# Kernel optimization log

Measured on AMD Instinct MI355X. Metric: run time of the kernel, lower is better.

## Reference

```python
import jax, jax.numpy as jnp
import numpy as np

D_MODEL = 4096
RANK = 16
BATCH = 4
SEQ = 4096


def setup_inputs() -> dict:
    key = jax.random.key(0)
    k_x, k_w, k_b, k_a, k_bb = jax.random.split(key, 5)
    x = jax.random.normal(k_x, (BATCH, SEQ, D_MODEL), dtype=jnp.float32)
    W = jax.random.normal(k_w, (D_MODEL, D_MODEL), dtype=jnp.float32) * 0.02
    bias = jax.random.normal(k_b, (D_MODEL,), dtype=jnp.float32) * 0.02
    A = jax.random.normal(k_a, (D_MODEL, RANK), dtype=jnp.float32) * 0.01
    B = jax.random.normal(k_bb, (RANK, D_MODEL), dtype=jnp.float32) * 0.01
    return {"x": x, "W": W, "bias": bias, "A": A, "B": B}


def reference(x, W, bias, A, B):
    # Faithful to the torch module: delta_W = A @ B; linear(x, W + delta_W, bias)
    # i.e. out = x @ (W + A @ B)^T + bias, with W: [d_out, d_in], x: [b, s, d_in].
    delta_W = A @ B                                   # [d_out, d_in]
    out = jnp.einsum("bsi,oi->bso", x, W + delta_W) + bias
    return out
```

## Files before the change

### kernel.cpp

```cpp
#include <hip/hip_runtime.h>
#include <stdint.h>


#define MDIM 16384
#define NDIM 4096
#define KDIM 4096
#define RANK 16
#define NT   (KDIM / 64)

typedef __bf16  bf16x8 __attribute__((ext_vector_type(8)));
typedef float   f32x4  __attribute__((ext_vector_type(4)));
typedef unsigned short u16x8 __attribute__((ext_vector_type(8)));

__device__ __forceinline__ unsigned short f2bf(float f) {
  union { float f; uint32_t u; } v; v.f = f;
  uint32_t r = v.u + 0x7FFFu + ((v.u >> 16) & 1u);
  return (unsigned short)(r >> 16);
}

__device__ __forceinline__ void gl16(const void* g, void* l) {
  __builtin_amdgcn_global_load_lds(
      (__attribute__((address_space(1))) void*)(g),
      (__attribute__((address_space(3))) void*)(l),
      16, 0, 0);
}

#define CAST_BLOCKS 32768
__global__ void prep_fused(const float* __restrict__ x,
                           const float* __restrict__ W,
                           const float* __restrict__ A,
                           const float* __restrict__ Bm,
                           unsigned short* __restrict__ xb,
                           unsigned short* __restrict__ Wp) {
  const int b = blockIdx.x;
  if (b < CAST_BLOCKS) {
    const size_t i = ((size_t)b * 256 + threadIdx.x) * 8;
    float4 a0 = *(const float4*)(x + i);
    float4 a1 = *(const float4*)(x + i + 4);
    u16x8 o;
    o[0] = f2bf(a0.x); o[1] = f2bf(a0.y); o[2] = f2bf(a0.z); o[3] = f2bf(a0.w);
    o[4] = f2bf(a1.x); o[5] = f2bf(a1.y); o[6] = f2bf(a1.z); o[7] = f2bf(a1.w);
    *(u16x8*)(xb + i) = o;
  } else {
    const size_t idx = ((size_t)(b - CAST_BLOCKS) * 256 + threadIdx.x) * 8;
    const int o  = (int)(idx >> 12);
    const int i0 = (int)(idx & 4095);
    float accv[8];
    {
      float4 w0 = *(const float4*)(W + (size_t)o * NDIM + i0);
      float4 w1 = *(const float4*)(W + (size_t)o * NDIM + i0 + 4);
      accv[0] = w0.x; accv[1] = w0.y; accv[2] = w0.z; accv[3] = w0.w;
      accv[4] = w1.x; accv[5] = w1.y; accv[6] = w1.z; accv[7] = w1.w;
    }
#pragma unroll
    for (int r = 0; r < RANK; ++r) {
      const float ar = A[o * RANK + r];
      float4 b0 = *(const float4*)(Bm + (size_t)r * NDIM + i0);
      float4 b1 = *(const float4*)(Bm + (size_t)r * NDIM + i0 + 4);
      accv[0] += ar * b0.x; accv[1] += ar * b0.y;
      accv[2] += ar * b0.z; accv[3] += ar * b0.w;
      accv[4] += ar * b1.x; accv[5] += ar * b1.y;
      accv[6] += ar * b1.z; accv[7] += ar * b1.w;
    }
    u16x8 ov;
#pragma unroll
    for (int j = 0; j < 8; ++j) ov[j] = f2bf(accv[j]);
    *(u16x8*)(Wp + idx) = ov;
  }
}

#define BARRIER  __builtin_amdgcn_s_barrier()
#define VMCNT8   asm volatile("s_waitcnt vmcnt(8)" ::: "memory")
#define WAITVM0  asm volatile("s_waitcnt vmcnt(0)" ::: "memory")
#define LGKMC_(n) asm volatile("s_waitcnt lgkmcnt(" #n ")" ::: "memory")
#define LGKMC(n) LGKMC_(n)
#define SCHEDB   __builtin_amdgcn_sched_barrier(0)
#define PRIO1    __builtin_amdgcn_s_setprio(1)
#define PRIO0    __builtin_amdgcn_s_setprio(0)

#define DSR(dst, addr, imm)                                                   \
  asm volatile("ds_read_b128 %0, %1 offset:%c2"                               \
               : "=v"(dst) : "v"(addr), "n"(imm) : "memory")

#define STAGE_A(buf, h, kt) do {                                              \
    const int kc_ = ((kt) < NT ? (kt) : NT - 1);                              \
    const unsigned short* g_ = agb + (size_t)((h) * 64) * KDIM + kc_ * 64;    \
    unsigned short* d_ = &sA[(buf)][0] + (h) * 8192 + t * 8;                  \
    gl16(g_, d_);                                                             \
    gl16(g_ + (size_t)128 * KDIM, d_ + 4096);                                 \
  } while (0)

#define STAGE_B(buf, h, kt) do {                                              \
    const int kc_ = ((kt) < NT ? (kt) : NT - 1);                              \
    const unsigned short* g_ = bgb + (size_t)((h) * 32) * KDIM + kc_ * 64;    \
    unsigned short* d_ = &sB[(buf)][0] + (h) * 8192 + t * 8;                  \
    gl16(g_, d_);                                                             \
    gl16(g_ + (size_t)128 * KDIM, d_ + 4096);                                 \
  } while (0)

#define LDA(buf, mh) do {                                                     \
    DSR(a[0][0], aAddr0, (buf)*32768 + (mh)*16384 + 0);                       \
    DSR(a[0][1], aAddr1, (buf)*32768 + (mh)*16384 + 0);                       \
    DSR(a[1][0], aAddr0, (buf)*32768 + (mh)*16384 + 2048);                    \
    DSR(a[1][1], aAddr1, (buf)*32768 + (mh)*16384 + 2048);                    \
    DSR(a[2][0], aAddr0, (buf)*32768 + (mh)*16384 + 4096);                    \
    DSR(a[2][1], aAddr1, (buf)*32768 + (mh)*16384 + 4096);                    \
    DSR(a[3][0], aAddr0, (buf)*32768 + (mh)*16384 + 6144);                    \
    DSR(a[3][1], aAddr1, (buf)*32768 + (mh)*16384 + 6144);                    \
  } while (0)

#define LDB(bb, buf, nh) do {                                                 \
    DSR(bb[0][0], bAddr0, (buf)*32768 + (nh)*16384 + 0);                      \
    DSR(bb[0][1], bAddr1, (buf)*32768 + (nh)*16384 + 0);                      \
    DSR(bb[1][0], bAddr0, (buf)*32768 + (nh)*16384 + 2048);                   \
    DSR(bb[1][1], bAddr1, (buf)*32768 + (nh)*16384 + 2048);                   \
  } while (0)

#define MMmi(mh, nh, mi, bb) do {                                             \
    _Pragma("unroll") for (int ni = 0; ni < 2; ++ni)                          \
    _Pragma("unroll") for (int kk = 0; kk < 2; ++kk)                          \
      acc[(mh)*4+(mi)][(nh)*2+ni] = __builtin_amdgcn_mfma_f32_16x16x32_bf16(  \
          a[mi][kk], bb[ni][kk], acc[(mh)*4+(mi)][(nh)*2+ni], 0, 0, 0);       \
  } while (0)

#define MMni(mh, nh, ni, bb) do {                                             \
    _Pragma("unroll") for (int mi = 0; mi < 4; ++mi)                          \
    _Pragma("unroll") for (int kk = 0; kk < 2; ++kk)                          \
      acc[(mh)*4+mi][(nh)*2+(ni)] = __builtin_amdgcn_mfma_f32_16x16x32_bf16(  \
          a[mi][kk], bb[ni][kk], acc[(mh)*4+mi][(nh)*2+(ni)], 0, 0, 0);       \
  } while (0)

#define MMfull(mh, nh, bb) do {                                               \
    _Pragma("unroll") for (int mi = 0; mi < 4; ++mi)                          \
    _Pragma("unroll") for (int ni = 0; ni < 2; ++ni)                          \
    _Pragma("unroll") for (int kk = 0; kk < 2; ++kk)                          \
      acc[(mh)*4+mi][(nh)*2+ni] = __builtin_amdgcn_mfma_f32_16x16x32_bf16(    \
          a[mi][kk], bb[ni][kk], acc[(mh)*4+mi][(nh)*2+ni], 0, 0, 0);         \
  } while (0)

#define PH_A(bb, mh, nh)                                                      \
    PRIO1; LGKMC(6); SCHEDB; MMmi(mh, nh, 0, bb);                             \
    LGKMC(4); SCHEDB; MMmi(mh, nh, 1, bb);                                    \
    LGKMC(2); SCHEDB; MMmi(mh, nh, 2, bb);                                    \
    LGKMC(0); SCHEDB; MMmi(mh, nh, 3, bb); PRIO0

#define PH_B(bb, mh, nh)                                                      \
    PRIO1; LGKMC(2); SCHEDB; MMni(mh, nh, 0, bb);                             \
    LGKMC(0); SCHEDB; MMni(mh, nh, 1, bb); PRIO0

__global__ __launch_bounds__(512, 2) void gemm256(
    const unsigned short* __restrict__ Xb,
    const unsigned short* __restrict__ Wp,
    const float* __restrict__ bias,
    float* __restrict__ out) {
  __shared__ __align__(16) unsigned short sA[2][256 * 64];
  __shared__ __align__(16) unsigned short sB[2][256 * 64];

  const int t  = threadIdx.x;
  const int l  = t & 63;
  const int w  = t >> 6;
  const int wm = w >> 2;
  const int wn = w & 3;

  const int bid = blockIdx.x;
  const int swz = (bid & 7) * (1024 / 8) + (bid >> 3);
  const int bm  = (swz >> 4) * 256;
  const int bn  = (swz & 15) * 256;

  const int sr  = t >> 3;
  const int ske = (((t & 7) * 16) ^ ((sr & 7) << 4)) >> 1;
  const unsigned short* agb = Xb + (size_t)(bm + sr) * KDIM + ske;
  const unsigned short* bgb = Wp + (size_t)(bn + (sr >> 5) * 64 + (sr & 31)) * KDIM + ske;

  const int lr   = l & 15;
  const int koff = (l >> 4) * 8;
  const int xorE = (lr & 7) << 3;
  const unsigned ldsA = (unsigned)(uintptr_t)&sA[0][0];
  const unsigned ldsB = (unsigned)(uintptr_t)&sB[0][0];
  const unsigned aAddr0 = ldsA + (unsigned)((wm * 64 + lr) * 128 + ((koff ^ xorE) * 2));
  const unsigned aAddr1 = ldsA + (unsigned)((wm * 64 + lr) * 128 + (((32 + koff) ^ xorE) * 2));
  const unsigned bAddr0 = ldsB + (unsigned)((wn * 32 + lr) * 128 + ((koff ^ xorE) * 2));
  const unsigned bAddr1 = ldsB + (unsigned)((wn * 32 + lr) * 128 + (((32 + koff) ^ xorE) * 2));

  bf16x8 a[4][2], b0[2][2], b1[2][2];
  f32x4 acc[8][4];
#pragma unroll
  for (int i = 0; i < 8; ++i)
#pragma unroll
    for (int j = 0; j < 4; ++j)
      acc[i][j] = f32x4{0.f, 0.f, 0.f, 0.f};

  STAGE_B(0, 0, 0); STAGE_A(0, 0, 0);
  STAGE_B(0, 1, 0); STAGE_A(0, 1, 0);
  STAGE_B(1, 0, 1); STAGE_A(1, 0, 1);
  VMCNT8;
  BARRIER;

  for (int it = 0; it < NT / 2; ++it) {
    const int E = it * 2;
    LDB(b0, 0, 0); LDA(0, 0);
    STAGE_B(1, 1, E + 1);
    VMCNT8; BARRIER;
    PH_A(b0, 0, 0);
    LDB(b1, 0, 1);
    STAGE_A(1, 1, E + 1);
    VMCNT8; BARRIER;
    PH_B(b1, 0, 1);
    LDA(0, 1);
    STAGE_B(0, 0, E + 2);
    VMCNT8; BARRIER;
    PH_A(b1, 1, 1);
    STAGE_A(0, 0, E + 2);
    VMCNT8; BARRIER;
    PRIO1; MMfull(1, 0, b0); PRIO0;
    LDB(b0, 1, 0); LDA(1, 0);
    STAGE_B(0, 1, E + 2);
    VMCNT8; BARRIER;
    PH_A(b0, 0, 0);
    LDB(b1, 1, 1);
    STAGE_A(0, 1, E + 2);
    VMCNT8; BARRIER;
    PH_B(b1, 0, 1);
    LDA(1, 1);
    STAGE_B(1, 0, E + 3);
    VMCNT8; BARRIER;
    PH_A(b1, 1, 1);
    STAGE_A(1, 0, E + 3);
    VMCNT8; BARRIER;
    PRIO1; MMfull(1, 0, b0); PRIO0;
  }

  LGKMC(0);
  WAITVM0;

#pragma unroll
  for (int mf = 0; mf < 8; ++mf) {
#pragma unroll
    for (int nf = 0; nf < 4; ++nf) {
      const int row = bm + wm * 128 + mf * 16 + (l >> 4) * 4;
      const int col = bn + wn * 64 + nf * 16 + lr;
      const float bv = bias[col];
#pragma unroll
      for (int r = 0; r < 4; ++r)
        out[(size_t)(row + r) * NDIM + col] = acc[mf][nf][r] + bv;
    }
  }
}

extern "C" void kernel_launch(void* const* d_in, const int* in_sizes, int n_in,
                              void* d_out, int out_size, void* d_ws, size_t ws_size,
                              hipStream_t stream) {
  const float* x    = (const float*)d_in[0];
  const float* W    = (const float*)d_in[1];
  const float* bias = (const float*)d_in[2];
  const float* A    = (const float*)d_in[3];
  const float* B    = (const float*)d_in[4];
  float* out        = (float*)d_out;

  unsigned short* Wp = (unsigned short*)d_ws;
  unsigned short* Xb = (unsigned short*)d_ws + (size_t)NDIM * KDIM;

  prep_fused<<<dim3(CAST_BLOCKS + 8192), 256, 0, stream>>>(x, W, A, B, Xb, Wp);
  gemm256<<<dim3((MDIM / 256) * (NDIM / 256)), 512, 0, stream>>>(Xb, Wp, bias, out);
}
```

Measured before the change: 583.3 us.

## Restructure GEMM main loop into two barrier phases per k-tile with deeper prefetch

Reorganizes the software-pipelined bf16 MFMA main loop from four barrier-separated phases per k-tile into two larger phases (16-MFMA and 8+full blocks). Global-to-LDS staging is regrouped so three quarter-tiles are issued together before one barrier, with adjusted vmcnt waits (6 and 2) and LDS fragment reads hoisted to the end of the previous phase. The aim is to cut barrier count and wait stalls while keeping loads overlapped with compute. The risk is weaker overlap or hazards if the new wait counts do not match the outstanding-load ordering.

```diff
diff --git a/kernel.cpp b/kernel.cpp
--- a/kernel.cpp
+++ b/kernel.cpp
@@ -70,7 +70,8 @@
 }
 
 #define BARRIER  __builtin_amdgcn_s_barrier()
-#define VMCNT8   asm volatile("s_waitcnt vmcnt(8)" ::: "memory")
+#define VMCNT6   asm volatile("s_waitcnt vmcnt(6)" ::: "memory")
+#define VMCNT2   asm volatile("s_waitcnt vmcnt(2)" ::: "memory")
 #define WAITVM0  asm volatile("s_waitcnt vmcnt(0)" ::: "memory")
 #define LGKMC_(n) asm volatile("s_waitcnt lgkmcnt(" #n ")" ::: "memory")
 #define LGKMC(n) LGKMC_(n)
@@ -138,15 +139,20 @@
           a[mi][kk], bb[ni][kk], acc[(mh)*4+mi][(nh)*2+ni], 0, 0, 0);         \
   } while (0)
 
-#define PH_A(bb, mh, nh)                                                      \
-    PRIO1; LGKMC(6); SCHEDB; MMmi(mh, nh, 0, bb);                             \
-    LGKMC(4); SCHEDB; MMmi(mh, nh, 1, bb);                                    \
-    LGKMC(2); SCHEDB; MMmi(mh, nh, 2, bb);                                    \
-    LGKMC(0); SCHEDB; MMmi(mh, nh, 3, bb); PRIO0
-
-#define PH_B(bb, mh, nh)                                                      \
-    PRIO1; LGKMC(2); SCHEDB; MMni(mh, nh, 0, bb);                             \
-    LGKMC(0); SCHEDB; MMni(mh, nh, 1, bb); PRIO0
+#define PH16(bb0, bb1)                                                        \
+    PRIO1; LGKMC(10); SCHEDB; MMmi(0, 0, 0, bb0);                             \
+    LGKMC(8);  SCHEDB; MMmi(0, 0, 1, bb0);                                    \
+    LGKMC(6);  SCHEDB; MMmi(0, 0, 2, bb0);                                    \
+    LGKMC(4);  SCHEDB; MMmi(0, 0, 3, bb0);                                    \
+    LGKMC(2);  SCHEDB; MMni(0, 1, 0, bb1);                                    \
+    LGKMC(0);  SCHEDB; MMni(0, 1, 1, bb1); PRIO0
+
+#define PH8(bb1, bb0)                                                         \
+    PRIO1; LGKMC(6); SCHEDB; MMmi(1, 1, 0, bb1);                              \
+    LGKMC(4); SCHEDB; MMmi(1, 1, 1, bb1);                                     \
+    LGKMC(2); SCHEDB; MMmi(1, 1, 2, bb1);                                     \
+    LGKMC(0); SCHEDB; MMmi(1, 1, 3, bb1);                                     \
+    MMfull(1, 0, bb0); PRIO0
 
 __global__ __launch_bounds__(512, 2) void gemm256(
     const unsigned short* __restrict__ Xb,
@@ -190,44 +196,29 @@
     for (int j = 0; j < 4; ++j)
       acc[i][j] = f32x4{0.f, 0.f, 0.f, 0.f};
 
-  STAGE_B(0, 0, 0); STAGE_A(0, 0, 0);
-  STAGE_B(0, 1, 0); STAGE_A(0, 1, 0);
-  STAGE_B(1, 0, 1); STAGE_A(1, 0, 1);
-  VMCNT8;
+  STAGE_B(0, 0, 0); STAGE_A(0, 0, 0); STAGE_B(0, 1, 0); STAGE_A(0, 1, 0);
+  WAITVM0;
   BARRIER;
+  LDB(b0, 0, 0); LDA(0, 0); LDB(b1, 0, 1);
 
   for (int it = 0; it < NT / 2; ++it) {
     const int E = it * 2;
-    LDB(b0, 0, 0); LDA(0, 0);
-    STAGE_B(1, 1, E + 1);
-    VMCNT8; BARRIER;
-    PH_A(b0, 0, 0);
-    LDB(b1, 0, 1);
+    STAGE_B(1, 0, E + 1); STAGE_A(1, 0, E + 1); STAGE_B(1, 1, E + 1);
+    VMCNT6; BARRIER;
+    PH16(b0, b1);
+    LDA(0, 1);
     STAGE_A(1, 1, E + 1);
-    VMCNT8; BARRIER;
-    PH_B(b1, 0, 1);
-    LDA(0, 1);
-    STAGE_B(0, 0, E + 2);
-    VMCNT8; BARRIER;
-    PH_A(b1, 1, 1);
-    STAGE_A(0, 0, E + 2);
-    VMCNT8; BARRIER;
-    PRIO1; MMfull(1, 0, b0); PRIO0;
-    LDB(b0, 1, 0); LDA(1, 0);
-    STAGE_B(0, 1, E + 2);
-    VMCNT8; BARRIER;
-    PH_A(b0, 0, 0);
-    LDB(b1, 1, 1);
+    VMCNT2; BARRIER;
+    PH8(b1, b0);
+    LDB(b0, 1, 0); LDA(1, 0); LDB(b1, 1, 1);
+    STAGE_B(0, 0, E + 2); STAGE_A(0, 0, E + 2); STAGE_B(0, 1, E + 2);
+    VMCNT6; BARRIER;
+    PH16(b0, b1);
+    LDA(1, 1);
     STAGE_A(0, 1, E + 2);
-    VMCNT8; BARRIER;
-    PH_B(b1, 0, 1);
-    LDA(1, 1);
-    STAGE_B(1, 0, E + 3);
-    VMCNT8; BARRIER;
-    PH_A(b1, 1, 1);
-    STAGE_A(1, 0, E + 3);
-    VMCNT8; BARRIER;
-    PRIO1; MMfull(1, 0, b0); PRIO0;
+    VMCNT2; BARRIER;
+    PH8(b1, b0);
+    LDB(b0, 0, 0); LDA(0, 0); LDB(b1, 0, 1);
   }
 
   LGKMC(0);
```

Measured after the change: 606.1 us. 1.04x slower.
